# Kernel optimization log

Measured on AMD Instinct MI355X. Metric: run time of the kernel, lower is better.

The kernel has to match this reference:

```python
import jax, jax.numpy as jnp
import numpy as np

N_HEAD = 8

def _l2norm(x, eps=1e-12):
    # F.normalize(p=2, dim=-1): x / max(||x||_2, eps)
    return x / jnp.maximum(jnp.linalg.norm(x, axis=-1, keepdims=True), eps)

def setup_inputs() -> dict:
    key = jax.random.key(0)
    ks = jax.random.split(key, 9)
    B, L, E = 2, 2048, 512
    s = 0.02
    return {
        "query": jax.random.normal(ks[0], (B, L, E), dtype=jnp.float32),
        "Wq": s * jax.random.normal(ks[1], (E, E), dtype=jnp.float32),
        "bq": jnp.zeros((E,), dtype=jnp.float32),
        "Wk": s * jax.random.normal(ks[2], (E, E), dtype=jnp.float32),
        "bk": jnp.zeros((E,), dtype=jnp.float32),
        "Wv": s * jax.random.normal(ks[3], (E, E), dtype=jnp.float32),
        "bv": jnp.zeros((E,), dtype=jnp.float32),
        "Wo": s * jax.random.normal(ks[4], (E, E), dtype=jnp.float32),
        "bo": jnp.zeros((E,), dtype=jnp.float32),
    }

def reference(query, Wq, bq, Wk, bk, Wv, bv, Wo, bo):
    B, L, E = query.shape
    H = N_HEAD
    hd = E // H
    # Faithful to torch: .view(tgt_len, bsz, E) is a RESHAPE, not a transpose.
    x = query.reshape(L, B, E)
    q = jax.nn.relu(x @ Wq.T + bq)
    k = jax.nn.relu(x @ Wk.T + bk)
    v = x @ Wv.T + bv
    q = _l2norm(q)
    k = _l2norm(k)
    # (L, B, E) -> (L, B*H, hd) -> (B*H, L, hd)
    q_ = q.reshape(L, B * H, hd).transpose(1, 0, 2)
    k_ = k.reshape(L, B * H, hd).transpose(1, 0, 2)
    v_ = v.reshape(L, B * H, hd).transpose(1, 0, 2)
    # Causal linear attention: cumulative outer-product of k,v then contract with q.
    kv = jnp.einsum('nld,nlm->nldm', k_, v_)      # [B*H, L, hd, hd]
    kv_cum = jnp.cumsum(kv, axis=1)
    out = jnp.einsum('nld,nldm->nlm', q_, kv_cum)  # [B*H, L, hd]
    out = out.transpose(1, 0, 2).reshape(L, B, E)
    out = out @ Wo.T + bo
    return out.reshape(B, L, E)
```

## Files before the change

### kernel.cpp

```cpp
#include <hip/hip_runtime.h>
#include <hip/hip_bf16.h>

typedef __attribute__((ext_vector_type(8))) short short8;
typedef __attribute__((ext_vector_type(4))) float f32x4;
using bf16 = __hip_bfloat16;

__device__ __forceinline__ unsigned short f2bf(float f) {
    unsigned u = __float_as_uint(f);
    u += 0x7fff + ((u >> 16) & 1);
    return (unsigned short)(u >> 16);
}
__device__ __forceinline__ float bf2f(unsigned short s) {
    return __uint_as_float(((unsigned)s) << 16);
}
__device__ __forceinline__ void gl_lds16(const unsigned short* g, unsigned short* l) {
    __builtin_amdgcn_global_load_lds(
        (const __attribute__((address_space(1))) unsigned int*)g,
        (__attribute__((address_space(3))) unsigned int*)l, 16, 0, 0);
}


__global__ __launch_bounds__(256) void pack_kernel(
    const float* __restrict__ X, const float* __restrict__ Wq, const float* __restrict__ Wk,
    const float* __restrict__ Wv, const float* __restrict__ Wo,
    bf16* __restrict__ Xp, bf16* __restrict__ Wqp, bf16* __restrict__ Wkp,
    bf16* __restrict__ Wvp, bf16* __restrict__ Wop, float* __restrict__ ssq)
{
    __shared__ __align__(16) unsigned short sm[4096];
    int id = blockIdx.x;
    int tid = threadIdx.x;
    if (id < 8) {
        int zi = id * 1024 + tid * 4;
        *(float4*)&ssq[zi] = make_float4(0.f, 0.f, 0.f, 0.f);
    }
    const float* src; unsigned short* dst; int g, sc;
    if (id < 512) { src = X; dst = (unsigned short*)Xp; g = id >> 3; sc = id & 7; }
    else {
        int t = id - 512; int wsel = t >> 6; int u = t & 63;
        g = u >> 3; sc = u & 7;
        src = (wsel == 0) ? Wq : ((wsel == 1) ? Wk : ((wsel == 2) ? Wv : Wo));
        dst = (unsigned short*)((wsel == 0) ? Wqp : ((wsel == 1) ? Wkp : ((wsel == 2) ? Wvp : Wop)));
    }
    int r = tid >> 2, kq = tid & 3;
    const float* sp = src + (size_t)(g * 64 + r) * 512 + sc * 64 + kq * 16;
    #pragma unroll
    for (int i = 0; i < 4; ++i) {
        float4 v = *(const float4*)(sp + i * 4);
        int kk = kq * 16 + i * 4;
        int sl = kk >> 3, el = kk & 7;
        ushort4 u4;
        u4.x = f2bf(v.x); u4.y = f2bf(v.y); u4.z = f2bf(v.z); u4.w = f2bf(v.w);
        *(ushort4*)&sm[(sl * 64 + r) * 8 + el] = u4;
    }
    __syncthreads();
    unsigned short* dp = dst + (size_t)g * 32768 + sc * 4096;
    *(uint4*)(dp + tid * 16)     = *(const uint4*)&sm[tid * 16];
    *(uint4*)(dp + tid * 16 + 8) = *(const uint4*)&sm[tid * 16 + 8];
}

__global__ __launch_bounds__(256) void qkv_gemm_kernel(
    const bf16* __restrict__ Xp,
    const bf16* __restrict__ W0p, const bf16* __restrict__ W1p, const bf16* __restrict__ W2p,
    const float* __restrict__ b0, const float* __restrict__ b1, const float* __restrict__ b2,
    bf16* __restrict__ O0, bf16* __restrict__ O1, bf16* __restrict__ O2,
    float* __restrict__ ssq)
{
    __shared__ __align__(16) unsigned short smem[24576];
    int z = blockIdx.z;
    const unsigned short* Wg = (const unsigned short*)((z == 0) ? W0p : ((z == 1) ? W1p : W2p));
    const float* bias = (z == 0) ? b0 : ((z == 1) ? b1 : b2);
    unsigned short* Out = (unsigned short*)((z == 0) ? O0 : ((z == 1) ? O1 : O2));
    const unsigned short* Ag = (const unsigned short*)Xp;

    int g  = blockIdx.x;
    int gB = blockIdx.y * 2;
    int m0 = g * 64;
    int n0 = blockIdx.y * 128;
    int tid = threadIdx.x;
    int lane = tid & 63;
    int w = tid >> 6;
    int wm = (w >> 1) * 32;
    int wn = (w & 1) * 64;
    int fr = lane & 15, qf = lane >> 4;

    f32x4 zero4 = {0.f, 0.f, 0.f, 0.f};
    f32x4 acc[2][4];
    #pragma unroll
    for (int t = 0; t < 2; ++t)
        #pragma unroll
        for (int u = 0; u < 4; ++u) acc[t][u] = zero4;

#define QKV_STAGE(buf, it) do {                                                             \
        unsigned short* As_ = smem + (buf) * 12288;                                         \
        unsigned short* Bs_ = As_ + 4096;                                                   \
        int s0_ = (it) * 8;                                                                 \
        gl_lds16(Ag + ((size_t)(g * 64 + s0_ + w * 2)     * 64 + lane) * 8, As_ + w * 1024);        \
        gl_lds16(Ag + ((size_t)(g * 64 + s0_ + w * 2 + 1) * 64 + lane) * 8, As_ + w * 1024 + 512);  \
        gl_lds16(Wg + ((size_t)((gB + (w >> 1)) * 64 + s0_ + (w & 1) * 4)     * 64 + lane) * 8, Bs_ + (w * 4)     * 512); \
        gl_lds16(Wg + ((size_t)((gB + (w >> 1)) * 64 + s0_ + (w & 1) * 4 + 1) * 64 + lane) * 8, Bs_ + (w * 4 + 1) * 512); \
        gl_lds16(Wg + ((size_t)((gB + (w >> 1)) * 64 + s0_ + (w & 1) * 4 + 2) * 64 + lane) * 8, Bs_ + (w * 4 + 2) * 512); \
        gl_lds16(Wg + ((size_t)((gB + (w >> 1)) * 64 + s0_ + (w & 1) * 4 + 3) * 64 + lane) * 8, Bs_ + (w * 4 + 3) * 512); \
    } while (0)

    int cur = 0;
    QKV_STAGE(0, 0);
    __syncthreads();
    for (int it = 0; it < 8; ++it) {
        if (it < 7) QKV_STAGE(cur ^ 1, it + 1);
        const unsigned short* As = smem + cur * 12288;
        const unsigned short* Bs = As + 4096;
        #pragma unroll
        for (int kk = 0; kk < 2; ++kk) {
            short8 af[2], bfr[4];
            #pragma unroll
            for (int t = 0; t < 2; ++t)
                af[t] = *(const short8*)&As[((kk * 4 + qf) * 64 + wm + t * 16 + fr) * 8];
            #pragma unroll
            for (int u = 0; u < 4; ++u)
                bfr[u] = *(const short8*)&Bs[(((w & 1) * 8 + kk * 4 + qf) * 64 + u * 16 + fr) * 8];
            #pragma unroll
            for (int t = 0; t < 2; ++t)
                #pragma unroll
                for (int u = 0; u < 4; ++u)
                    acc[t][u] = __builtin_amdgcn_mfma_f32_16x16x32_bf16(af[t], bfr[u], acc[t][u], 0, 0, 0);
        }
        __syncthreads();
        cur ^= 1;
    }
#undef QKV_STAGE

    bool relu = (z < 2);
    int rb = qf * 4;
    #pragma unroll
    for (int t = 0; t < 2; ++t)
        #pragma unroll
        for (int u = 0; u < 4; ++u) {
            float bv = bias[n0 + wn + u * 16 + fr];
            #pragma unroll
            for (int r = 0; r < 4; ++r) {
                float v = acc[t][u][r] + bv;
                if (relu) v = fmaxf(v, 0.f);
                acc[t][u][r] = v;
            }
        }
    if (relu) {
        #pragma unroll
        for (int t = 0; t < 2; ++t)
            #pragma unroll
            for (int r = 0; r < 4; ++r) {
                float s = 0.f;
                #pragma unroll
                for (int u = 0; u < 4; ++u) s += acc[t][u][r] * acc[t][u][r];
                #pragma unroll
                for (int off = 1; off < 16; off <<= 1) s += __shfl_xor(s, off, 64);
                if (fr == 0) atomicAdd(&ssq[z * 4096 + m0 + wm + t * 16 + rb + r], s);
            }
    }
    #pragma unroll
    for (int t = 0; t < 2; ++t)
        #pragma unroll
        for (int u = 0; u < 4; ++u)
            #pragma unroll
            for (int r = 0; r < 4; ++r)
                smem[(wm + t * 16 + rb + r) * 128 + wn + u * 16 + fr] = f2bf(acc[t][u][r]);
    __syncthreads();
    #pragma unroll
    for (int rep = 0; rep < 4; ++rep) {
        int idx8 = rep * 256 + tid;
        int row = idx8 >> 4, col8 = (idx8 & 15) * 8;
        *(uint4*)(Out + (size_t)(m0 + row) * 512 + n0 + col8) = *(const uint4*)&smem[row * 128 + col8];
    }
}

__global__ __launch_bounds__(256) void chunk_kv_kernel(
    const bf16* __restrict__ Kb, const bf16* __restrict__ Vb,
    const float* __restrict__ ssq, float* __restrict__ ScT, bf16* __restrict__ Vt_g)
{
    int n = blockIdx.x >> 5, c = blockIdx.x & 31;
    int b = n >> 3, h = n & 7;
    __shared__ float Ks[64 * 64];
    __shared__ float Vs[64 * 64];
    const unsigned short* Kg = (const unsigned short*)Kb;
    const unsigned short* Vg = (const unsigned short*)Vb;
    int tid = threadIdx.x;
    int td = tid >> 4, tm = tid & 15;
    int d0 = td * 4, m0 = tm * 4;
    #pragma unroll
    for (int rep = 0; rep < 4; ++rep) {
        int idx = rep * 1024 + tid * 4;
        int j = idx >> 6, d = idx & 63;
        int grow = (c * 64 + j) * 2 + b;
        ushort4 ku = *(const ushort4*)&Kg[(size_t)grow * 512 + h * 64 + d];
        ushort4 vu = *(const ushort4*)&Vg[(size_t)grow * 512 + h * 64 + d];
        float rk = 1.f / fmaxf(sqrtf(ssq[4096 + grow]), 1e-12f);
        *(float4*)&Ks[j * 64 + d] = make_float4(bf2f(ku.x), bf2f(ku.y), bf2f(ku.z), bf2f(ku.w));
        *(float4*)&Vs[j * 64 + d] = make_float4(bf2f(vu.x) * rk, bf2f(vu.y) * rk,
                                                bf2f(vu.z) * rk, bf2f(vu.w) * rk);
    }
    __syncthreads();
    float acc[4][4] = {};
    for (int j = 0; j < 64; ++j) {
        float4 kv = *(const float4*)&Ks[j * 64 + d0];
        float4 vv = *(const float4*)&Vs[j * 64 + m0];
        acc[0][0] += kv.x*vv.x; acc[0][1] += kv.x*vv.y; acc[0][2] += kv.x*vv.z; acc[0][3] += kv.x*vv.w;
        acc[1][0] += kv.y*vv.x; acc[1][1] += kv.y*vv.y; acc[1][2] += kv.y*vv.z; acc[1][3] += kv.y*vv.w;
        acc[2][0] += kv.z*vv.x; acc[2][1] += kv.z*vv.y; acc[2][2] += kv.z*vv.z; acc[2][3] += kv.z*vv.w;
        acc[3][0] += kv.w*vv.x; acc[3][1] += kv.w*vv.y; acc[3][2] += kv.w*vv.z; acc[3][3] += kv.w*vv.w;
    }
    int vm = tid & 63, vj0 = (tid >> 6) * 16;
    unsigned short tmp[16];
    #pragma unroll
    for (int i = 0; i < 16; ++i) tmp[i] = f2bf(Vs[(vj0 + i) * 64 + vm]);
    size_t vtoff = (size_t)n * 131072 + (size_t)vm * 2048 + c * 64 + vj0;
    *(uint4*)((unsigned short*)Vt_g + vtoff)     = *(uint4*)&tmp[0];
    *(uint4*)((unsigned short*)Vt_g + vtoff + 8) = *(uint4*)&tmp[8];

    float* outp = ScT + (size_t)blockIdx.x * 4096;
    #pragma unroll
    for (int j2 = 0; j2 < 4; ++j2) {
        float4 o4 = make_float4(acc[0][j2], acc[1][j2], acc[2][j2], acc[3][j2]);
        *(float4*)&outp[(m0 + j2) * 64 + d0] = o4;
    }
}

__global__ __launch_bounds__(256) void prefix_kernel(const float* __restrict__ ScT, bf16* __restrict__ SpT)
{
    int n = blockIdx.x >> 4;
    int idx = ((blockIdx.x & 15) << 8) + threadIdx.x;
    size_t base = (size_t)n * 131072 + idx;
    unsigned short* sp = (unsigned short*)SpT;
    float run = 0.f;
    #pragma unroll
    for (int c = 0; c < 32; ++c) {
        size_t off = base + (size_t)c * 4096;
        sp[off] = f2bf(run);
        run += ScT[off];
    }
}

__global__ __launch_bounds__(256) void attn_kernel(
    const bf16* __restrict__ Qb, const bf16* __restrict__ Kb,
    const bf16* __restrict__ Vt_g, const bf16* __restrict__ SpT_g,
    const float* __restrict__ ssq, bf16* __restrict__ AOb)
{
    int n = blockIdx.x >> 5, c = blockIdx.x & 31;
    int b = n >> 3, h = n & 7;
    __shared__ __align__(16) unsigned short Qs[64 * 72];
    __shared__ __align__(16) unsigned short Ks[64 * 72];
    __shared__ __align__(16) unsigned short Vt[64 * 72];
    __shared__ __align__(16) unsigned short Ps[4 * 16 * 40];
    int tid = threadIdx.x;
    int lane = tid & 63;
    int w = tid >> 6;
    int fr = lane & 15, q = lane >> 4;

    const unsigned short* Qg = (const unsigned short*)Qb;
    const unsigned short* Kg = (const unsigned short*)Kb;
    const unsigned short* Vg = (const unsigned short*)Vt_g;

    #pragma unroll
    for (int rep = 0; rep < 2; ++rep) {
        int idx = rep * 256 + tid;
        int l = idx >> 3, dc = (idx & 7) * 8;
        size_t goff = (size_t)((c * 64 + l) * 2 + b) * 512 + h * 64 + dc;
        *(uint4*)&Qs[l * 72 + dc] = *(const uint4*)(Qg + goff);
        *(uint4*)&Ks[l * 72 + dc] = *(const uint4*)(Kg + goff);
        int m = l, jc = dc;
        *(uint4*)&Vt[m * 72 + jc] =
            *(const uint4*)(Vg + (size_t)n * 131072 + (size_t)m * 2048 + c * 64 + jc);
    }
    __syncthreads();

    short8 qf[2];
    #pragma unroll
    for (int kh = 0; kh < 2; ++kh)
        qf[kh] = *(const short8*)&Qs[(w * 16 + fr) * 72 + kh * 32 + q * 8];

    f32x4 zero4 = {0.f, 0.f, 0.f, 0.f};
    f32x4 oacc[4];
    #pragma unroll
    for (int mt = 0; mt < 4; ++mt) oacc[mt] = zero4;

    const unsigned short* spg = (const unsigned short*)SpT_g + (size_t)blockIdx.x * 4096;
    #pragma unroll
    for (int mt = 0; mt < 4; ++mt) {
        #pragma unroll
        for (int kh = 0; kh < 2; ++kh) {
            short8 sf = *(const short8*)&spg[(mt * 16 + fr) * 64 + kh * 32 + q * 8];
            oacc[mt] = __builtin_amdgcn_mfma_f32_16x16x32_bf16(qf[kh], sf, oacc[mt], 0, 0, 0);
        }
    }

    unsigned short* myPs = &Ps[w * 640];
    int rbase = q * 4;
    int njt = (w >> 1) + 1;
    for (int jt = 0; jt < njt; ++jt) {
        f32x4 pacc[2];
        pacc[0] = zero4; pacc[1] = zero4;
        #pragma unroll
        for (int jt16 = 0; jt16 < 2; ++jt16) {
            #pragma unroll
            for (int kh = 0; kh < 2; ++kh) {
                short8 kf = *(const short8*)&Ks[(jt * 32 + jt16 * 16 + fr) * 72 + kh * 32 + q * 8];
                pacc[jt16] = __builtin_amdgcn_mfma_f32_16x16x32_bf16(qf[kh], kf, pacc[jt16], 0, 0, 0);
            }
        }
        bool diag = (jt == njt - 1);
        int lloc = w * 16 + rbase;
        #pragma unroll
        for (int jt16 = 0; jt16 < 2; ++jt16)
            #pragma unroll
            for (int r = 0; r < 4; ++r) {
                int jl = jt * 32 + jt16 * 16 + fr;
                float pv = pacc[jt16][r];
                if (diag && jl > lloc + r) pv = 0.f;
                myPs[(rbase + r) * 40 + jt16 * 16 + fr] = f2bf(pv);
            }
        short8 pf = *(const short8*)&myPs[fr * 40 + q * 8];
        #pragma unroll
        for (int mt = 0; mt < 4; ++mt) {
            short8 vf = *(const short8*)&Vt[(mt * 16 + fr) * 72 + jt * 32 + q * 8];
            oacc[mt] = __builtin_amdgcn_mfma_f32_16x16x32_bf16(pf, vf, oacc[mt], 0, 0, 0);
        }
    }

    float rqv[4];
    #pragma unroll
    for (int r = 0; r < 4; ++r) {
        int flat = (c * 64 + w * 16 + rbase + r) * 2 + b;
        rqv[r] = 1.f / fmaxf(sqrtf(ssq[flat]), 1e-12f);
    }
    __syncthreads();
    #pragma unroll
    for (int mt = 0; mt < 4; ++mt)
        #pragma unroll
        for (int r = 0; r < 4; ++r)
            Qs[(w * 16 + rbase + r) * 64 + mt * 16 + fr] = f2bf(oacc[mt][r] * rqv[r]);
    __syncthreads();
    #pragma unroll
    for (int rep = 0; rep < 2; ++rep) {
        int idx8 = rep * 256 + tid;
        int sl = idx8 >> 6, l = idx8 & 63;
        *(uint4*)((unsigned short*)AOb +
                  (size_t)(((c * 2 + b) * 64 + h * 8 + sl) * 64 + l) * 8) =
            *(const uint4*)&Qs[l * 64 + sl * 8];
    }
}

__global__ __launch_bounds__(256) void oproj_kernel(
    const bf16* __restrict__ A, const bf16* __restrict__ Wop,
    const float* __restrict__ bias, float* __restrict__ Out)
{
    __shared__ __align__(16) unsigned short smem[16384];
    const unsigned short* Ag = (const unsigned short*)A;
    const unsigned short* Wg = (const unsigned short*)Wop;
    int gp = blockIdx.x;
    int gy = blockIdx.y;
    int n0 = gy * 64;
    int tid = threadIdx.x;
    int lane = tid & 63;
    int w = tid >> 6;
    int fr = lane & 15, qf = lane >> 4;
    int wm = (w >> 1) * 32;
    int wn = (w & 1) * 32;

    f32x4 zero4 = {0.f, 0.f, 0.f, 0.f};
    f32x4 acc[2][2];
    acc[0][0] = zero4; acc[0][1] = zero4; acc[1][0] = zero4; acc[1][1] = zero4;

#define OPJ_STAGE(buf, it) do {                                                             \
        unsigned short* As_ = smem + (buf) * 8192;                                          \
        unsigned short* Bs_ = As_ + 4096;                                                   \
        int s0_ = (it) * 8;                                                                 \
        gl_lds16(Ag + ((size_t)(gp * 64 + s0_ + w * 2)     * 64 + lane) * 8, As_ + w * 1024);        \
        gl_lds16(Ag + ((size_t)(gp * 64 + s0_ + w * 2 + 1) * 64 + lane) * 8, As_ + w * 1024 + 512);  \
        gl_lds16(Wg + ((size_t)(gy * 64 + s0_ + w * 2)     * 64 + lane) * 8, Bs_ + w * 1024);        \
        gl_lds16(Wg + ((size_t)(gy * 64 + s0_ + w * 2 + 1) * 64 + lane) * 8, Bs_ + w * 1024 + 512);  \
    } while (0)

    int cur = 0;
    OPJ_STAGE(0, 0);
    __syncthreads();
    for (int it = 0; it < 8; ++it) {
        if (it < 7) OPJ_STAGE(cur ^ 1, it + 1);
        const unsigned short* As = smem + cur * 8192;
        const unsigned short* Bs = As + 4096;
        #pragma unroll
        for (int kk = 0; kk < 2; ++kk) {
            short8 af[2], bf[2];
            #pragma unroll
            for (int t = 0; t < 2; ++t)
                af[t] = *(const short8*)&As[((kk * 4 + qf) * 64 + wm + t * 16 + fr) * 8];
            #pragma unroll
            for (int u = 0; u < 2; ++u)
                bf[u] = *(const short8*)&Bs[((kk * 4 + qf) * 64 + wn + u * 16 + fr) * 8];
            #pragma unroll
            for (int t = 0; t < 2; ++t)
                #pragma unroll
                for (int u = 0; u < 2; ++u)
                    acc[t][u] = __builtin_amdgcn_mfma_f32_16x16x32_bf16(af[t], bf[u], acc[t][u], 0, 0, 0);
        }
        __syncthreads();
        cur ^= 1;
    }
#undef OPJ_STAGE

    int rb = qf * 4;
    float* Cf = (float*)smem;
    #pragma unroll
    for (int t = 0; t < 2; ++t)
        #pragma unroll
        for (int u = 0; u < 2; ++u) {
            float bv = bias[n0 + wn + u * 16 + fr];
            #pragma unroll
            for (int r = 0; r < 4; ++r)
                Cf[(wm + t * 16 + rb + r) * 64 + wn + u * 16 + fr] = acc[t][u][r] + bv;
        }
    __syncthreads();
    int cbase = (gp >> 1) * 128, bb = gp & 1;
    #pragma unroll
    for (int rep = 0; rep < 4; ++rep) {
        int idx = rep * 256 + tid;
        int l2 = idx >> 4, c4 = (idx & 15) * 4;
        *(float4*)(Out + (size_t)(cbase + l2 * 2 + bb) * 512 + n0 + c4) = *(const float4*)&Cf[l2 * 64 + c4];
    }
}

extern "C" void kernel_launch(void* const* d_in, const int* in_sizes, int n_in,
                              void* d_out, int out_size, void* d_ws, size_t ws_size,
                              hipStream_t stream)
{
    (void)in_sizes; (void)n_in; (void)out_size; (void)ws_size;
    const float* x  = (const float*)d_in[0];
    const float* Wq = (const float*)d_in[1];
    const float* bq = (const float*)d_in[2];
    const float* Wk = (const float*)d_in[3];
    const float* bk = (const float*)d_in[4];
    const float* Wv = (const float*)d_in[5];
    const float* bv = (const float*)d_in[6];
    const float* Wo = (const float*)d_in[7];
    const float* bo = (const float*)d_in[8];
    float* out = (float*)d_out;

    float* ssq = (float*)d_ws;
    bf16* Xp  = (bf16*)(ssq + 8192);
    bf16* Wqp = Xp + 2097152;
    bf16* Wkp = Wqp + 262144;
    bf16* Wvp = Wkp + 262144;
    bf16* Wop = Wvp + 262144;
    bf16* Qb  = Wop + 262144;
    bf16* Kb  = Qb + 2097152;
    bf16* Vb  = Kb + 2097152;
    bf16* Vt  = Vb + 2097152;
    bf16* AOb = Vt + 2097152;
    bf16* SpT = AOb + 2097152;
    float* ScT = (float*)(SpT + 2097152);

    pack_kernel<<<768, 256, 0, stream>>>(x, Wq, Wk, Wv, Wo, Xp, Wqp, Wkp, Wvp, Wop, ssq);
    qkv_gemm_kernel<<<dim3(64, 4, 3), 256, 0, stream>>>(Xp, Wqp, Wkp, Wvp, bq, bk, bv, Qb, Kb, Vb, ssq);
    chunk_kv_kernel<<<dim3(512), 256, 0, stream>>>(Kb, Vb, ssq, ScT, Vt);
    prefix_kernel<<<dim3(256), 256, 0, stream>>>(ScT, SpT);
    attn_kernel<<<dim3(512), 256, 0, stream>>>(Qb, Kb, Vt, SpT, ssq, AOb);
    oproj_kernel<<<dim3(64, 8), 256, 0, stream>>>(AOb, Wop, bo, out);
}
```

Measured before the change: 116.7 us.

## Fuse QKV projections per tile, drop prefix kernel, sum chunk states in attention

The QKV GEMM now computes all three projections in one block over a 64x64 tile, so each X tile is loaded once and reused for Wq, Wk and Wv instead of being reloaded across a z grid dimension. The separate prefix-scan kernel is removed: chunk_kv writes per-chunk KV states in bf16, and each attention block sums the states of all earlier chunks itself. This saves one launch and the fp32 intermediate traffic, but gives the attention kernel work that grows with chunk index (up to 31 redundant reads per block, unbalanced across blocks) and adds bf16 rounding to each partial state before summation.

```diff
diff --git a/kernel.cpp b/kernel.cpp
--- a/kernel.cpp
+++ b/kernel.cpp
@@ -65,41 +65,40 @@
     bf16* __restrict__ O0, bf16* __restrict__ O1, bf16* __restrict__ O2,
     float* __restrict__ ssq)
 {
-    __shared__ __align__(16) unsigned short smem[24576];
-    int z = blockIdx.z;
-    const unsigned short* Wg = (const unsigned short*)((z == 0) ? W0p : ((z == 1) ? W1p : W2p));
-    const float* bias = (z == 0) ? b0 : ((z == 1) ? b1 : b2);
-    unsigned short* Out = (unsigned short*)((z == 0) ? O0 : ((z == 1) ? O1 : O2));
-    const unsigned short* Ag = (const unsigned short*)Xp;
-
-    int g  = blockIdx.x;
-    int gB = blockIdx.y * 2;
-    int m0 = g * 64;
-    int n0 = blockIdx.y * 128;
+    __shared__ __align__(16) unsigned short smem[32768];
+    const unsigned short* Ag  = (const unsigned short*)Xp;
+    const unsigned short* W0g = (const unsigned short*)W0p;
+    const unsigned short* W1g = (const unsigned short*)W1p;
+    const unsigned short* W2g = (const unsigned short*)W2p;
+    int g = blockIdx.x, gy = blockIdx.y;
+    int m0 = g * 64, n0 = gy * 64;
     int tid = threadIdx.x;
     int lane = tid & 63;
     int w = tid >> 6;
     int wm = (w >> 1) * 32;
-    int wn = (w & 1) * 64;
+    int wn = (w & 1) * 32;
     int fr = lane & 15, qf = lane >> 4;
 
     f32x4 zero4 = {0.f, 0.f, 0.f, 0.f};
-    f32x4 acc[2][4];
-    #pragma unroll
-    for (int t = 0; t < 2; ++t)
-        #pragma unroll
-        for (int u = 0; u < 4; ++u) acc[t][u] = zero4;
-
-#define QKV_STAGE(buf, it) do {                                                             \
-        unsigned short* As_ = smem + (buf) * 12288;                                         \
-        unsigned short* Bs_ = As_ + 4096;                                                   \
-        int s0_ = (it) * 8;                                                                 \
-        gl_lds16(Ag + ((size_t)(g * 64 + s0_ + w * 2)     * 64 + lane) * 8, As_ + w * 1024);        \
-        gl_lds16(Ag + ((size_t)(g * 64 + s0_ + w * 2 + 1) * 64 + lane) * 8, As_ + w * 1024 + 512);  \
-        gl_lds16(Wg + ((size_t)((gB + (w >> 1)) * 64 + s0_ + (w & 1) * 4)     * 64 + lane) * 8, Bs_ + (w * 4)     * 512); \
-        gl_lds16(Wg + ((size_t)((gB + (w >> 1)) * 64 + s0_ + (w & 1) * 4 + 1) * 64 + lane) * 8, Bs_ + (w * 4 + 1) * 512); \
-        gl_lds16(Wg + ((size_t)((gB + (w >> 1)) * 64 + s0_ + (w & 1) * 4 + 2) * 64 + lane) * 8, Bs_ + (w * 4 + 2) * 512); \
-        gl_lds16(Wg + ((size_t)((gB + (w >> 1)) * 64 + s0_ + (w & 1) * 4 + 3) * 64 + lane) * 8, Bs_ + (w * 4 + 3) * 512); \
+    f32x4 acc[3][2][2];
+    #pragma unroll
+    for (int z = 0; z < 3; ++z)
+        #pragma unroll
+        for (int t = 0; t < 2; ++t)
+            #pragma unroll
+            for (int u = 0; u < 2; ++u) acc[z][t][u] = zero4;
+
+#define QKV_STAGE(buf, it) do {                                                              \
+        unsigned short* bb = smem + (buf) * 16384;                                           \
+        int s0_ = (it) * 8 + w * 2;                                                          \
+        gl_lds16(Ag  + ((size_t)(g  * 64 + s0_)     * 64 + lane) * 8, bb + (w * 2)     * 512);        \
+        gl_lds16(Ag  + ((size_t)(g  * 64 + s0_ + 1) * 64 + lane) * 8, bb + (w * 2 + 1) * 512);        \
+        gl_lds16(W0g + ((size_t)(gy * 64 + s0_)     * 64 + lane) * 8, bb + 4096  + (w * 2)     * 512); \
+        gl_lds16(W0g + ((size_t)(gy * 64 + s0_ + 1) * 64 + lane) * 8, bb + 4096  + (w * 2 + 1) * 512); \
+        gl_lds16(W1g + ((size_t)(gy * 64 + s0_)     * 64 + lane) * 8, bb + 8192  + (w * 2)     * 512); \
+        gl_lds16(W1g + ((size_t)(gy * 64 + s0_ + 1) * 64 + lane) * 8, bb + 8192  + (w * 2 + 1) * 512); \
+        gl_lds16(W2g + ((size_t)(gy * 64 + s0_)     * 64 + lane) * 8, bb + 12288 + (w * 2)     * 512); \
+        gl_lds16(W2g + ((size_t)(gy * 64 + s0_ + 1) * 64 + lane) * 8, bb + 12288 + (w * 2 + 1) * 512); \
     } while (0)
 
     int cur = 0;
@@ -107,74 +106,83 @@
     __syncthreads();
     for (int it = 0; it < 8; ++it) {
         if (it < 7) QKV_STAGE(cur ^ 1, it + 1);
-        const unsigned short* As = smem + cur * 12288;
-        const unsigned short* Bs = As + 4096;
+        const unsigned short* As = smem + cur * 16384;
         #pragma unroll
         for (int kk = 0; kk < 2; ++kk) {
-            short8 af[2], bfr[4];
-            #pragma unroll
-            for (int t = 0; t < 2; ++t)
-                af[t] = *(const short8*)&As[((kk * 4 + qf) * 64 + wm + t * 16 + fr) * 8];
-            #pragma unroll
-            for (int u = 0; u < 4; ++u)
-                bfr[u] = *(const short8*)&Bs[(((w & 1) * 8 + kk * 4 + qf) * 64 + u * 16 + fr) * 8];
+            int ks = (kk * 4 + qf) * 64;
+            short8 af[2];
+            af[0] = *(const short8*)&As[(ks + wm + fr) * 8];
+            af[1] = *(const short8*)&As[(ks + wm + 16 + fr) * 8];
+            #pragma unroll
+            for (int z = 0; z < 3; ++z) {
+                const unsigned short* Bs = As + 4096 + z * 4096;
+                short8 bf0 = *(const short8*)&Bs[(ks + wn + fr) * 8];
+                short8 bf1 = *(const short8*)&Bs[(ks + wn + 16 + fr) * 8];
+                acc[z][0][0] = __builtin_amdgcn_mfma_f32_16x16x32_bf16(af[0], bf0, acc[z][0][0], 0, 0, 0);
+                acc[z][0][1] = __builtin_amdgcn_mfma_f32_16x16x32_bf16(af[0], bf1, acc[z][0][1], 0, 0, 0);
+                acc[z][1][0] = __builtin_amdgcn_mfma_f32_16x16x32_bf16(af[1], bf0, acc[z][1][0], 0, 0, 0);
+                acc[z][1][1] = __builtin_amdgcn_mfma_f32_16x16x32_bf16(af[1], bf1, acc[z][1][1], 0, 0, 0);
+            }
+        }
+        __syncthreads();
+        cur ^= 1;
+    }
+#undef QKV_STAGE
+
+    int rb = qf * 4;
+    #pragma unroll
+    for (int z = 0; z < 3; ++z) {
+        const float* bias = (z == 0) ? b0 : ((z == 1) ? b1 : b2);
+        #pragma unroll
+        for (int u = 0; u < 2; ++u) {
+            float bv = bias[n0 + wn + u * 16 + fr];
             #pragma unroll
             for (int t = 0; t < 2; ++t)
                 #pragma unroll
-                for (int u = 0; u < 4; ++u)
-                    acc[t][u] = __builtin_amdgcn_mfma_f32_16x16x32_bf16(af[t], bfr[u], acc[t][u], 0, 0, 0);
-        }
-        __syncthreads();
-        cur ^= 1;
-    }
-#undef QKV_STAGE
-
-    bool relu = (z < 2);
-    int rb = qf * 4;
-    #pragma unroll
-    for (int t = 0; t < 2; ++t)
-        #pragma unroll
-        for (int u = 0; u < 4; ++u) {
-            float bv = bias[n0 + wn + u * 16 + fr];
+                for (int r = 0; r < 4; ++r) {
+                    float v = acc[z][t][u][r] + bv;
+                    if (z < 2) v = fmaxf(v, 0.f);
+                    acc[z][t][u][r] = v;
+                }
+        }
+    }
+    #pragma unroll
+    for (int z = 0; z < 2; ++z)
+        #pragma unroll
+        for (int t = 0; t < 2; ++t)
             #pragma unroll
             for (int r = 0; r < 4; ++r) {
-                float v = acc[t][u][r] + bv;
-                if (relu) v = fmaxf(v, 0.f);
-                acc[t][u][r] = v;
-            }
-        }
-    if (relu) {
-        #pragma unroll
-        for (int t = 0; t < 2; ++t)
-            #pragma unroll
-            for (int r = 0; r < 4; ++r) {
-                float s = 0.f;
-                #pragma unroll
-                for (int u = 0; u < 4; ++u) s += acc[t][u][r] * acc[t][u][r];
+                float s = acc[z][t][0][r] * acc[z][t][0][r] + acc[z][t][1][r] * acc[z][t][1][r];
                 #pragma unroll
                 for (int off = 1; off < 16; off <<= 1) s += __shfl_xor(s, off, 64);
                 if (fr == 0) atomicAdd(&ssq[z * 4096 + m0 + wm + t * 16 + rb + r], s);
             }
-    }
-    #pragma unroll
-    for (int t = 0; t < 2; ++t)
-        #pragma unroll
-        for (int u = 0; u < 4; ++u)
-            #pragma unroll
-            for (int r = 0; r < 4; ++r)
-                smem[(wm + t * 16 + rb + r) * 128 + wn + u * 16 + fr] = f2bf(acc[t][u][r]);
-    __syncthreads();
-    #pragma unroll
-    for (int rep = 0; rep < 4; ++rep) {
-        int idx8 = rep * 256 + tid;
-        int row = idx8 >> 4, col8 = (idx8 & 15) * 8;
-        *(uint4*)(Out + (size_t)(m0 + row) * 512 + n0 + col8) = *(const uint4*)&smem[row * 128 + col8];
+    #pragma unroll
+    for (int z = 0; z < 3; ++z)
+        #pragma unroll
+        for (int t = 0; t < 2; ++t)
+            #pragma unroll
+            for (int u = 0; u < 2; ++u)
+                #pragma unroll
+                for (int r = 0; r < 4; ++r)
+                    smem[z * 4096 + (wm + t * 16 + rb + r) * 64 + wn + u * 16 + fr] = f2bf(acc[z][t][u][r]);
+    __syncthreads();
+    unsigned short* O0s = (unsigned short*)O0;
+    unsigned short* O1s = (unsigned short*)O1;
+    unsigned short* O2s = (unsigned short*)O2;
+    #pragma unroll
+    for (int rep = 0; rep < 6; ++rep) {
+        int idx = rep * 256 + tid;
+        int z = idx >> 9, rem = idx & 511;
+        int row = rem >> 3, col8 = (rem & 7) * 8;
+        unsigned short* Oz = (z == 0) ? O0s : ((z == 1) ? O1s : O2s);
+        *(uint4*)(Oz + (size_t)(m0 + row) * 512 + n0 + col8) = *(const uint4*)&smem[z * 4096 + row * 64 + col8];
     }
 }
 
 __global__ __launch_bounds__(256) void chunk_kv_kernel(
     const bf16* __restrict__ Kb, const bf16* __restrict__ Vb,
-    const float* __restrict__ ssq, float* __restrict__ ScT, bf16* __restrict__ Vt_g)
+    const float* __restrict__ ssq, bf16* __restrict__ ScT, bf16* __restrict__ Vt_g)
 {
     int n = blockIdx.x >> 5, c = blockIdx.x & 31;
     int b = n >> 3, h = n & 7;
@@ -215,32 +223,19 @@
     *(uint4*)((unsigned short*)Vt_g + vtoff)     = *(uint4*)&tmp[0];
     *(uint4*)((unsigned short*)Vt_g + vtoff + 8) = *(uint4*)&tmp[8];
 
-    float* outp = ScT + (size_t)blockIdx.x * 4096;
+    unsigned short* outp = (unsigned short*)ScT + (size_t)blockIdx.x * 4096;
     #pragma unroll
     for (int j2 = 0; j2 < 4; ++j2) {
-        float4 o4 = make_float4(acc[0][j2], acc[1][j2], acc[2][j2], acc[3][j2]);
-        *(float4*)&outp[(m0 + j2) * 64 + d0] = o4;
-    }
-}
-
-__global__ __launch_bounds__(256) void prefix_kernel(const float* __restrict__ ScT, bf16* __restrict__ SpT)
-{
-    int n = blockIdx.x >> 4;
-    int idx = ((blockIdx.x & 15) << 8) + threadIdx.x;
-    size_t base = (size_t)n * 131072 + idx;
-    unsigned short* sp = (unsigned short*)SpT;
-    float run = 0.f;
-    #pragma unroll
-    for (int c = 0; c < 32; ++c) {
-        size_t off = base + (size_t)c * 4096;
-        sp[off] = f2bf(run);
-        run += ScT[off];
+        ushort4 o4;
+        o4.x = f2bf(acc[0][j2]); o4.y = f2bf(acc[1][j2]);
+        o4.z = f2bf(acc[2][j2]); o4.w = f2bf(acc[3][j2]);
+        *(ushort4*)&outp[(m0 + j2) * 64 + d0] = o4;
     }
 }
 
 __global__ __launch_bounds__(256) void attn_kernel(
     const bf16* __restrict__ Qb, const bf16* __restrict__ Kb,
-    const bf16* __restrict__ Vt_g, const bf16* __restrict__ SpT_g,
+    const bf16* __restrict__ Vt_g, const bf16* __restrict__ ScT_g,
     const float* __restrict__ ssq, bf16* __restrict__ AOb)
 {
     int n = blockIdx.x >> 5, c = blockIdx.x & 31;
@@ -269,25 +264,47 @@
         *(uint4*)&Vt[m * 72 + jc] =
             *(const uint4*)(Vg + (size_t)n * 131072 + (size_t)m * 2048 + c * 64 + jc);
     }
-    __syncthreads();
-
-    short8 qf[2];
+
+    float sacc[4][2][8];
+    #pragma unroll
+    for (int mt = 0; mt < 4; ++mt)
+        #pragma unroll
+        for (int kh = 0; kh < 2; ++kh)
+            #pragma unroll
+            for (int e = 0; e < 8; ++e) sacc[mt][kh][e] = 0.f;
+    const unsigned short* scb = (const unsigned short*)ScT_g + (size_t)n * 131072;
+    for (int cp = 0; cp < c; ++cp) {
+        const unsigned short* pl = scb + cp * 4096;
+        #pragma unroll
+        for (int mt = 0; mt < 4; ++mt)
+            #pragma unroll
+            for (int kh = 0; kh < 2; ++kh) {
+                uint4 uu = *(const uint4*)&pl[(mt * 16 + fr) * 64 + kh * 32 + q * 8];
+                const unsigned short* us = (const unsigned short*)&uu;
+                #pragma unroll
+                for (int e = 0; e < 8; ++e) sacc[mt][kh][e] += bf2f(us[e]);
+            }
+    }
+    __syncthreads();
+
+    short8 qfr[2];
     #pragma unroll
     for (int kh = 0; kh < 2; ++kh)
-        qf[kh] = *(const short8*)&Qs[(w * 16 + fr) * 72 + kh * 32 + q * 8];
+        qfr[kh] = *(const short8*)&Qs[(w * 16 + fr) * 72 + kh * 32 + q * 8];
 
     f32x4 zero4 = {0.f, 0.f, 0.f, 0.f};
     f32x4 oacc[4];
     #pragma unroll
     for (int mt = 0; mt < 4; ++mt) oacc[mt] = zero4;
 
-    const unsigned short* spg = (const unsigned short*)SpT_g + (size_t)blockIdx.x * 4096;
     #pragma unroll
     for (int mt = 0; mt < 4; ++mt) {
         #pragma unroll
         for (int kh = 0; kh < 2; ++kh) {
-            short8 sf = *(const short8*)&spg[(mt * 16 + fr) * 64 + kh * 32 + q * 8];
-            oacc[mt] = __builtin_amdgcn_mfma_f32_16x16x32_bf16(qf[kh], sf, oacc[mt], 0, 0, 0);
+            short8 sf;
+            #pragma unroll
+            for (int e = 0; e < 8; ++e) sf[e] = (short)f2bf(sacc[mt][kh][e]);
+            oacc[mt] = __builtin_amdgcn_mfma_f32_16x16x32_bf16(qfr[kh], sf, oacc[mt], 0, 0, 0);
         }
     }
 
@@ -302,7 +319,7 @@
             #pragma unroll
             for (int kh = 0; kh < 2; ++kh) {
                 short8 kf = *(const short8*)&Ks[(jt * 32 + jt16 * 16 + fr) * 72 + kh * 32 + q * 8];
-                pacc[jt16] = __builtin_amdgcn_mfma_f32_16x16x32_bf16(qf[kh], kf, pacc[jt16], 0, 0, 0);
+                pacc[jt16] = __builtin_amdgcn_mfma_f32_16x16x32_bf16(qfr[kh], kf, pacc[jt16], 0, 0, 0);
             }
         }
         bool diag = (jt == njt - 1);
@@ -387,18 +404,18 @@
         const unsigned short* Bs = As + 4096;
         #pragma unroll
         for (int kk = 0; kk < 2; ++kk) {
-            short8 af[2], bf[2];
+            short8 af[2], bfx[2];
             #pragma unroll
             for (int t = 0; t < 2; ++t)
                 af[t] = *(const short8*)&As[((kk * 4 + qf) * 64 + wm + t * 16 + fr) * 8];
             #pragma unroll
             for (int u = 0; u < 2; ++u)
-                bf[u] = *(const short8*)&Bs[((kk * 4 + qf) * 64 + wn + u * 16 + fr) * 8];
+                bfx[u] = *(const short8*)&Bs[((kk * 4 + qf) * 64 + wn + u * 16 + fr) * 8];
             #pragma unroll
             for (int t = 0; t < 2; ++t)
                 #pragma unroll
                 for (int u = 0; u < 2; ++u)
-                    acc[t][u] = __builtin_amdgcn_mfma_f32_16x16x32_bf16(af[t], bf[u], acc[t][u], 0, 0, 0);
+                    acc[t][u] = __builtin_amdgcn_mfma_f32_16x16x32_bf16(af[t], bfx[u], acc[t][u], 0, 0, 0);
         }
         __syncthreads();
         cur ^= 1;
@@ -453,13 +470,11 @@
     bf16* Vb  = Kb + 2097152;
     bf16* Vt  = Vb + 2097152;
     bf16* AOb = Vt + 2097152;
-    bf16* SpT = AOb + 2097152;
-    float* ScT = (float*)(SpT + 2097152);
+    bf16* ScT = AOb + 2097152;
 
     pack_kernel<<<768, 256, 0, stream>>>(x, Wq, Wk, Wv, Wo, Xp, Wqp, Wkp, Wvp, Wop, ssq);
-    qkv_gemm_kernel<<<dim3(64, 4, 3), 256, 0, stream>>>(Xp, Wqp, Wkp, Wvp, bq, bk, bv, Qb, Kb, Vb, ssq);
+    qkv_gemm_kernel<<<dim3(64, 8), 256, 0, stream>>>(Xp, Wqp, Wkp, Wvp, bq, bk, bv, Qb, Kb, Vb, ssq);
     chunk_kv_kernel<<<dim3(512), 256, 0, stream>>>(Kb, Vb, ssq, ScT, Vt);
-    prefix_kernel<<<dim3(256), 256, 0, stream>>>(ScT, SpT);
-    attn_kernel<<<dim3(512), 256, 0, stream>>>(Qb, Kb, Vt, SpT, ssq, AOb);
+    attn_kernel<<<dim3(512), 256, 0, stream>>>(Qb, Kb, Vt, ScT, ssq, AOb);
     oproj_kernel<<<dim3(64, 8), 256, 0, stream>>>(AOb, Wop, bo, out);
 }
```

Result: slower. 165.7 us (+42.0%).
